# Performance work log

Measured on AMD Instinct MI355X. Metric: run time of the kernel, lower is better.

Reference implementation:

```python
import jax, jax.numpy as jnp
import numpy as np

D_MODEL = 2048
N_HEADS = 16
HEAD_DIM = D_MODEL // N_HEADS
CLIP_QKV = 6.0
LN_EPS = 1e-5


def _layernorm(x, g, b):
    mu = jnp.mean(x, axis=-1, keepdims=True)
    var = jnp.mean(jnp.square(x - mu), axis=-1, keepdims=True)
    return (x - mu) * jax.lax.rsqrt(var + LN_EPS) * g + b


def setup_inputs() -> dict:
    key = jax.random.key(0)
    ks = jax.random.split(key, 8)
    B, S = 2, 2048
    x = jax.random.normal(ks[0], (B, S, D_MODEL), dtype=jnp.float32)
    attn_bias = jax.random.normal(ks[1], (1, N_HEADS, 1, S), dtype=jnp.float32)
    key_padding_mask = jnp.ones((B, S), dtype=bool)
    Wqkv_w = jax.random.normal(ks[2], (3 * D_MODEL, D_MODEL), dtype=jnp.float32) * 0.02
    Wqkv_b = jnp.zeros((3 * D_MODEL,), dtype=jnp.float32)
    q_ln_g = jnp.ones((D_MODEL,), dtype=jnp.float32)
    q_ln_b = jnp.zeros((D_MODEL,), dtype=jnp.float32)
    k_ln_g = jnp.ones((D_MODEL,), dtype=jnp.float32)
    k_ln_b = jnp.zeros((D_MODEL,), dtype=jnp.float32)
    out_w = jax.random.normal(ks[3], (D_MODEL, D_MODEL), dtype=jnp.float32) * 0.02
    out_b = jnp.zeros((D_MODEL,), dtype=jnp.float32)
    return {
        'x': x, 'attn_bias': attn_bias, 'key_padding_mask': key_padding_mask,
        'Wqkv_w': Wqkv_w, 'Wqkv_b': Wqkv_b,
        'q_ln_g': q_ln_g, 'q_ln_b': q_ln_b, 'k_ln_g': k_ln_g, 'k_ln_b': k_ln_b,
        'out_w': out_w, 'out_b': out_b,
    }


def reference(x, attn_bias, key_padding_mask, Wqkv_w, Wqkv_b,
              q_ln_g, q_ln_b, k_ln_g, k_ln_b, out_w, out_b):
    B, S, _ = x.shape
    # Fused QKV projection + clip
    qkv = jnp.einsum('bsd,ed->bse', x, Wqkv_w) + Wqkv_b
    qkv = jnp.clip(qkv, -CLIP_QKV, CLIP_QKV)
    q, k, v = jnp.split(qkv, 3, axis=-1)
    # QK LayerNorm over full d_model
    q = _layernorm(q, q_ln_g, q_ln_b)
    k = _layernorm(k, k_ln_g, k_ln_b)
    # [b, s, d_model] -> [b, h, s, head_dim]
    q = q.reshape(B, S, N_HEADS, HEAD_DIM).transpose(0, 2, 1, 3)
    k = k.reshape(B, S, N_HEADS, HEAD_DIM).transpose(0, 2, 1, 3)
    v = v.reshape(B, S, N_HEADS, HEAD_DIM).transpose(0, 2, 1, 3)
    scale = 1.0 / np.sqrt(HEAD_DIM).astype(np.float32)
    scores = jnp.einsum('bhqd,bhkd->bhqk', q, k) * scale  # [b, h, s, s]
    scores = scores + attn_bias
    neg_inf = jnp.array(-jnp.inf, dtype=scores.dtype)
    scores = jnp.where(key_padding_mask[:, None, None, :], scores, neg_inf)
    causal = jnp.tril(jnp.ones((S, S), dtype=bool))
    scores = jnp.where(causal[None, None, :, :], scores, neg_inf)
    probs = jax.nn.softmax(scores, axis=-1)
    ctx = jnp.einsum('bhqk,bhkd->bhqd', probs, v)
    ctx = ctx.transpose(0, 2, 1, 3).reshape(B, S, D_MODEL)
    out = jnp.einsum('bsd,ed->bse', ctx, out_w) + out_b
    return out
```

## Files before the change

kernel.cpp:

```cpp
#include <hip/hip_runtime.h>

typedef unsigned short u16;
typedef unsigned int u32;
typedef __bf16 bf16x8 __attribute__((ext_vector_type(8)));
typedef float f32x4 __attribute__((ext_vector_type(4)));

#define DEV static __device__ __forceinline__

constexpr int D_MODEL = 2048;
constexpr int N_HEADS = 16;
constexpr int HEAD_DIM = 128;
constexpr int BB = 2;
constexpr int S = 2048;
constexpr int NTOK = BB * S;
constexpr int E3 = 3 * D_MODEL;
constexpr float CLIP_QKV = 6.0f;
constexpr float LN_EPS = 1e-5f;
constexpr float NEG_BIG = -30000.0f;

DEV u16 f2bf(float f) {
    u32 u = __float_as_uint(f);
    u = (u + 0x7FFFu + ((u >> 16) & 1u)) >> 16;
    return (u16)u;
}
DEV float bf2f(u16 h) { return __uint_as_float(((u32)h) << 16); }

DEV void stage8_f32(const float* __restrict__ src, u16* __restrict__ dst) {
    const float4 f0 = *reinterpret_cast<const float4*>(src);
    const float4 f1 = *reinterpret_cast<const float4*>(src + 4);
    u16 h[8] = {f2bf(f0.x), f2bf(f0.y), f2bf(f0.z), f2bf(f0.w),
                f2bf(f1.x), f2bf(f1.y), f2bf(f1.z), f2bf(f1.w)};
    *reinterpret_cast<uint4*>(dst) = *reinterpret_cast<const uint4*>(h);
}

DEV void gload16(const u16* g, u16* l) {
    __builtin_amdgcn_global_load_lds(
        (const __attribute__((address_space(1))) void*)g,
        (__attribute__((address_space(3))) void*)l, 16, 0, 0);
}

__global__ __launch_bounds__(256)
void k_cvt(const float* __restrict__ s, u16* __restrict__ d, int n8) {
    const int i = blockIdx.x * 256 + threadIdx.x;
    if (i < n8) stage8_f32(s + (size_t)i * 8, d + (size_t)i * 8);
}

template<bool DO_CLIP, bool OUT32>
__global__ __launch_bounds__(256)
void k_gemm_bt(const u16* __restrict__ A, const u16* __restrict__ Bm,
               const float* __restrict__ bias, void* __restrict__ Cp,
               int M, int N, int K) {
    __shared__ __align__(16) u16 As[128 * 32];
    __shared__ __align__(16) u16 Bs[128 * 32];

    const int tid = threadIdx.x;
    const int lane = tid & 63, w = tid >> 6;
    const int quad = lane >> 4, l16 = lane & 15;
    const int wm = w >> 1, wn = w & 1;
    const int m0 = blockIdx.y * 128, n0 = blockIdx.x * 128;

    f32x4 acc[4][4] = {};

    for (int k0 = 0; k0 < K; k0 += 32) {
        __syncthreads();
        #pragma unroll
        for (int j = 0; j < 2; ++j) {
            const int c = w * 128 + j * 64 + lane;
            const int row = c >> 2, cc = c & 3;
            gload16(A  + (size_t)(m0 + row) * K + k0 + cc * 8, &As[c * 8]);
            gload16(Bm + (size_t)(n0 + row) * K + k0 + cc * 8, &Bs[c * 8]);
        }
        __syncthreads();

        bf16x8 af[4], bfv[4];
        #pragma unroll
        for (int mt = 0; mt < 4; ++mt)
            af[mt] = *reinterpret_cast<const bf16x8*>(&As[(wm * 64 + mt * 16 + l16) * 32 + quad * 8]);
        #pragma unroll
        for (int nt = 0; nt < 4; ++nt)
            bfv[nt] = *reinterpret_cast<const bf16x8*>(&Bs[(wn * 64 + nt * 16 + l16) * 32 + quad * 8]);
        #pragma unroll
        for (int mt = 0; mt < 4; ++mt)
            #pragma unroll
            for (int nt = 0; nt < 4; ++nt)
                acc[mt][nt] = __builtin_amdgcn_mfma_f32_16x16x32_bf16(af[mt], bfv[nt], acc[mt][nt], 0, 0, 0);
    }

    #pragma unroll
    for (int mt = 0; mt < 4; ++mt) {
        const int row = m0 + wm * 64 + mt * 16 + quad * 4;
        #pragma unroll
        for (int nt = 0; nt < 4; ++nt) {
            const int col = n0 + wn * 64 + nt * 16 + l16;
            const float bv = bias[col];
            #pragma unroll
            for (int r = 0; r < 4; ++r) {
                float v = acc[mt][nt][r] + bv;
                if (DO_CLIP) v = fminf(CLIP_QKV, fmaxf(-CLIP_QKV, v));
                if (OUT32)
                    ((float*)Cp)[(size_t)(row + r) * N + col] = v;
                else
                    ((u16*)Cp)[(size_t)(row + r) * N + col] = f2bf(v);
            }
        }
    }
}

template<bool DO_CLIP, bool OUT32>
__global__ __launch_bounds__(512, 2)
void k_gemm256(const u16* __restrict__ A, const u16* __restrict__ Bm,
               const float* __restrict__ bias, void* __restrict__ Cp,
               int M, int N, int K) {
    __shared__ __align__(16) u16 lds[2][2][2][256 * 32];

    const int tid = threadIdx.x;
    const int lane = tid & 63, w = tid >> 6;
    const int quad = lane >> 4, l16 = lane & 15;
    const int wm = w >> 2, wn = w & 3;

    const int nwg = gridDim.x;
    const int bid = blockIdx.x;
    const int cpx = nwg >> 3;
    const int swz = (bid & 7) * cpx + (bid >> 3);
    const int gx = N >> 8;
    const int bx = swz % gx, by = swz / gx;
    const int m0 = by << 8, n0 = bx << 8;
    const int NT = K >> 6;

    u32 offA[2], offB[2];
    int loff[2];
    #pragma unroll
    for (int i = 0; i < 2; ++i) {
        const int c = i * 512 + w * 64 + lane;
        const int row = c >> 2;
        const int colb = ((c & 3) ^ ((row >> 1) & 3)) << 4;
        offA[i] = (u32)(m0 + row) * (u32)K + (u32)(colb >> 1);
        offB[i] = (u32)(n0 + row) * (u32)K + (u32)(colb >> 1);
        loff[i] = c * 8;
    }

    auto STAGE = [&](int buf, int op, int kh, int kt) {
        const u16* g = op ? Bm : A;
        const u32* of = op ? offB : offA;
        u16* l = lds[buf][op][kh];
        #pragma unroll
        for (int i = 0; i < 2; ++i)
            gload16(g + (size_t)of[i] + (size_t)(kt + kh * 32), l + loff[i]);
    };

    bf16x8 af[4], bfr[4];
    auto LDA = [&](int buf, int kh, int qm) {
        const u16* base = lds[buf][0][kh];
        #pragma unroll
        for (int mt = 0; mt < 4; ++mt) {
            const int row = wm * 128 + qm * 64 + mt * 16 + l16;
            af[mt] = *reinterpret_cast<const bf16x8*>(
                base + row * 32 + ((quad ^ ((row >> 1) & 3)) << 3));
        }
    };
    auto LDB = [&](int buf, int kh) {
        const u16* base = lds[buf][1][kh];
        #pragma unroll
        for (int nt = 0; nt < 4; ++nt) {
            const int row = wn * 64 + nt * 16 + l16;
            bfr[nt] = *reinterpret_cast<const bf16x8*>(
                base + row * 32 + ((quad ^ ((row >> 1) & 3)) << 3));
        }
    };

    f32x4 acc[2][4][4] = {};
    auto MM = [&](f32x4 (&ac)[4][4]) {
        __builtin_amdgcn_s_setprio(1);
        #pragma unroll
        for (int mt = 0; mt < 4; ++mt)
            #pragma unroll
            for (int nt = 0; nt < 4; ++nt)
                ac[mt][nt] = __builtin_amdgcn_mfma_f32_16x16x32_bf16(
                    af[mt], bfr[nt], ac[mt][nt], 0, 0, 0);
        __builtin_amdgcn_s_setprio(0);
    };

    STAGE(0, 0, 0, 0); STAGE(0, 1, 0, 0); STAGE(0, 0, 1, 0); STAGE(0, 1, 1, 0);
    if (NT > 1) {
        STAGE(1, 1, 0, 64); STAGE(1, 0, 0, 64); STAGE(1, 1, 1, 64);
        asm volatile("s_waitcnt vmcnt(6)" ::: "memory");
    } else {
        asm volatile("s_waitcnt vmcnt(0)" ::: "memory");
    }
    __builtin_amdgcn_s_barrier();
    __builtin_amdgcn_sched_barrier(0);

    for (int t = 0; t < NT; ++t) {
        const int p = t & 1;
        const int kt2 = (t + 2) << 6;

        LDA(p, 0, 0); LDB(p, 0);
        if (t + 1 < NT) STAGE(p ^ 1, 0, 1, (t + 1) << 6);
        __builtin_amdgcn_s_barrier();
        asm volatile("s_waitcnt lgkmcnt(0)");
        MM(acc[0]);
        __builtin_amdgcn_s_barrier();

        LDA(p, 0, 1);
        if (t + 2 < NT) STAGE(p, 1, 0, kt2);
        __builtin_amdgcn_s_barrier();
        asm volatile("s_waitcnt lgkmcnt(0)");
        MM(acc[1]);
        __builtin_amdgcn_s_barrier();

        LDA(p, 1, 0); LDB(p, 1);
        if (t + 2 < NT) STAGE(p, 0, 0, kt2);
        __builtin_amdgcn_s_barrier();
        asm volatile("s_waitcnt lgkmcnt(0)");
        MM(acc[0]);
        __builtin_amdgcn_s_barrier();

        LDA(p, 1, 1);
        if (t + 2 < NT) STAGE(p, 1, 1, kt2);
        __builtin_amdgcn_s_barrier();
        asm volatile("s_waitcnt lgkmcnt(0)");
        MM(acc[1]);
        if (t + 2 < NT)      asm volatile("s_waitcnt vmcnt(6)" ::: "memory");
        else if (t + 1 < NT) asm volatile("s_waitcnt vmcnt(0)" ::: "memory");
        __builtin_amdgcn_s_barrier();
        __builtin_amdgcn_sched_barrier(0);
    }

    #pragma unroll
    for (int qm = 0; qm < 2; ++qm)
        #pragma unroll
        for (int mt = 0; mt < 4; ++mt) {
            const int row = m0 + wm * 128 + qm * 64 + mt * 16 + quad * 4;
            #pragma unroll
            for (int nt = 0; nt < 4; ++nt) {
                const int col = n0 + wn * 64 + nt * 16 + l16;
                const float bv = bias[col];
                #pragma unroll
                for (int r = 0; r < 4; ++r) {
                    float v = acc[qm][mt][nt][r] + bv;
                    if (DO_CLIP) v = fminf(CLIP_QKV, fmaxf(-CLIP_QKV, v));
                    if (OUT32)
                        ((float*)Cp)[(size_t)(row + r) * N + col] = v;
                    else
                        ((u16*)Cp)[(size_t)(row + r) * N + col] = f2bf(v);
                }
            }
        }
}

__global__ __launch_bounds__(256)
void k_ln(const u16* __restrict__ qkvb,
          const float* __restrict__ gq, const float* __restrict__ bq,
          const float* __restrict__ gk, const float* __restrict__ bk,
          u16* __restrict__ qh, u16* __restrict__ kh) {
    __shared__ float red[8];
    const int tok = blockIdx.x;
    const int b = tok >> 11, s = tok & (S - 1);
    const int tid = threadIdx.x, lane = tid & 63, w = tid >> 6;

    #pragma unroll
    for (int part = 0; part < 2; ++part) {
        const int c0 = tid * 8;
        const u16* src = qkvb + (size_t)tok * E3 + part * D_MODEL + c0;
        u16 hx[8];
        *reinterpret_cast<uint4*>(hx) = *reinterpret_cast<const uint4*>(src);
        float x[8], sum = 0.f, sq = 0.f;
        #pragma unroll
        for (int j = 0; j < 8; ++j) { x[j] = bf2f(hx[j]); sum += x[j]; sq += x[j] * x[j]; }
        #pragma unroll
        for (int off = 1; off < 64; off <<= 1) {
            sum += __shfl_xor(sum, off, 64);
            sq  += __shfl_xor(sq,  off, 64);
        }
        __syncthreads();
        if (lane == 0) { red[w] = sum; red[4 + w] = sq; }
        __syncthreads();
        sum = red[0] + red[1] + red[2] + red[3];
        sq  = red[4] + red[5] + red[6] + red[7];
        const float mean = sum * (1.0f / D_MODEL);
        const float var  = fmaxf(sq * (1.0f / D_MODEL) - mean * mean, 0.0f);
        const float rstd = rsqrtf(var + LN_EPS);
        const float* g  = part ? gk : gq;
        const float* be = part ? bk : bq;
        u16 o[8];
        #pragma unroll
        for (int j = 0; j < 8; ++j)
            o[j] = f2bf((x[j] - mean) * rstd * g[c0 + j] + be[c0 + j]);
        const int h = c0 >> 7, d = c0 & (HEAD_DIM - 1);
        u16* dst = (part ? kh : qh) + ((size_t)((b * N_HEADS + h) * S + s)) * HEAD_DIM + d;
        *reinterpret_cast<uint4*>(dst) = *reinterpret_cast<uint4*>(o);
    }
}

__global__ __launch_bounds__(256)
void k_vtrans(const u16* __restrict__ qkvb, u16* __restrict__ vt) {
    constexpr int LDT = 136;
    __shared__ __align__(16) u16 tile[64 * LDT];
    const int blk = blockIdx.x;
    const int st = blk & 31, h = (blk >> 5) & 15, b = blk >> 9;
    const int s0 = st * 64;
    const int tid = threadIdx.x;

    #pragma unroll
    for (int i = 0; i < 4; ++i) {
        const int chunk = tid + i * 256;
        const int row = chunk >> 4, c8 = (chunk & 15) * 8;
        const u16* src = qkvb + (size_t)(b * S + s0 + row) * E3 + 2 * D_MODEL + h * HEAD_DIM + c8;
        *reinterpret_cast<uint4*>(&tile[row * LDT + c8]) = *reinterpret_cast<const uint4*>(src);
    }
    __syncthreads();
    #pragma unroll
    for (int i = 0; i < 4; ++i) {
        const int chunk = tid + i * 256;
        const int d = chunk >> 3, s8 = (chunk & 7) * 8;
        u16 o[8];
        #pragma unroll
        for (int j = 0; j < 8; ++j) o[j] = tile[(s8 + j) * LDT + d];
        u16* dst = vt + ((size_t)(b * N_HEADS + h) * HEAD_DIM + d) * S + s0 + s8;
        *reinterpret_cast<uint4*>(dst) = *reinterpret_cast<uint4*>(o);
    }
}

__global__ __launch_bounds__(256)
void k_attn(const u16* __restrict__ qh, const u16* __restrict__ kh,
            const u16* __restrict__ vt, const float* __restrict__ bias,
            u16* __restrict__ ctx) {
    constexpr int BQ = 128, BKV = 64;
    constexpr int LDK = 136;
    constexpr int LDV = 72;
    constexpr int LDP = 72;
    __shared__ __align__(16) u16 Ks[64 * LDK];
    __shared__ __align__(16) u16 Vs[128 * LDV];
    __shared__ __align__(16) u16 Ps[128 * LDP];

    const int blk = blockIdx.x;
    const int bh = blk & 31;
    const int qi = 15 - (blk >> 5);
    const int b = bh >> 4, h = bh & 15;
    const int q0 = qi * BQ;

    const int tid = threadIdx.x, lane = tid & 63, w = tid >> 6;
    const int quad = lane >> 4, l16 = lane & 15;

    const size_t bhS = (size_t)(b * N_HEADS + h) * S;
    const u16* Qt = qh + (bhS + q0) * HEAD_DIM;
    const u16* Kt = kh + bhS * HEAD_DIM;
    const u16* Vt = vt + (size_t)(b * N_HEADS + h) * HEAD_DIM * S;

    bf16x8 aq[2][4];
    #pragma unroll
    for (int mt = 0; mt < 2; ++mt)
        #pragma unroll
        for (int ks = 0; ks < 4; ++ks)
            aq[mt][ks] = *reinterpret_cast<const bf16x8*>(
                Qt + (size_t)(w * 32 + mt * 16 + l16) * HEAD_DIM + ks * 32 + quad * 8);

    f32x4 o[2][8] = {};
    float m_i[2][4], l_i[2][4];
    #pragma unroll
    for (int mt = 0; mt < 2; ++mt)
        #pragma unroll
        for (int r = 0; r < 4; ++r) { m_i[mt][r] = NEG_BIG; l_i[mt][r] = 0.f; }

    const float scale = 0.08838834764831845f;
    const int nkv = 2 * (qi + 1);

    for (int t = 0; t < nkv; ++t) {
        const int k0 = t * BKV;
        __syncthreads();
        #pragma unroll
        for (int i = 0; i < 4; ++i) {
            const int chunk = tid + i * 256;
            const int key = chunk >> 4, c8 = (chunk & 15) * 8;
            *reinterpret_cast<uint4*>(&Ks[key * LDK + c8]) =
                *reinterpret_cast<const uint4*>(Kt + (size_t)(k0 + key) * HEAD_DIM + c8);
        }
        #pragma unroll
        for (int i = 0; i < 4; ++i) {
            const int chunk = tid + i * 256;
            const int d = chunk >> 3, s8 = (chunk & 7) * 8;
            *reinterpret_cast<uint4*>(&Vs[d * LDV + s8]) =
                *reinterpret_cast<const uint4*>(Vt + (size_t)d * S + k0 + s8);
        }
        __syncthreads();

        f32x4 sc[2][4] = {};
        #pragma unroll
        for (int ks = 0; ks < 4; ++ks) {
            bf16x8 bk[4];
            #pragma unroll
            for (int nt = 0; nt < 4; ++nt)
                bk[nt] = *reinterpret_cast<const bf16x8*>(&Ks[(nt * 16 + l16) * LDK + ks * 32 + quad * 8]);
            #pragma unroll
            for (int mt = 0; mt < 2; ++mt)
                #pragma unroll
                for (int nt = 0; nt < 4; ++nt)
                    sc[mt][nt] = __builtin_amdgcn_mfma_f32_16x16x32_bf16(aq[mt][ks], bk[nt], sc[mt][nt], 0, 0, 0);
        }

        float bv[4];
        #pragma unroll
        for (int nt = 0; nt < 4; ++nt) bv[nt] = bias[h * S + k0 + nt * 16 + l16];
        const bool need_mask = (t >= 2 * qi);
        #pragma unroll
        for (int mt = 0; mt < 2; ++mt)
            #pragma unroll
            for (int nt = 0; nt < 4; ++nt) {
                const int kpos = k0 + nt * 16 + l16;
                #pragma unroll
                for (int r = 0; r < 4; ++r) {
                    float v = sc[mt][nt][r] * scale + bv[nt];
                    if (need_mask) {
                        const int qpos = q0 + w * 32 + mt * 16 + quad * 4 + r;
                        if (kpos > qpos) v = NEG_BIG;
                    }
                    sc[mt][nt][r] = v;
                }
            }

        #pragma unroll
        for (int mt = 0; mt < 2; ++mt)
            #pragma unroll
            for (int r = 0; r < 4; ++r) {
                float mx = fmaxf(fmaxf(sc[mt][0][r], sc[mt][1][r]), fmaxf(sc[mt][2][r], sc[mt][3][r]));
                mx = fmaxf(mx, __shfl_xor(mx, 1, 64));
                mx = fmaxf(mx, __shfl_xor(mx, 2, 64));
                mx = fmaxf(mx, __shfl_xor(mx, 4, 64));
                mx = fmaxf(mx, __shfl_xor(mx, 8, 64));
                const float mnew = fmaxf(m_i[mt][r], mx);
                const float alpha = __expf(m_i[mt][r] - mnew);
                float rs = 0.f;
                #pragma unroll
                for (int nt = 0; nt < 4; ++nt) {
                    const float p = __expf(sc[mt][nt][r] - mnew);
                    sc[mt][nt][r] = p;
                    rs += p;
                }
                rs += __shfl_xor(rs, 1, 64);
                rs += __shfl_xor(rs, 2, 64);
                rs += __shfl_xor(rs, 4, 64);
                rs += __shfl_xor(rs, 8, 64);
                l_i[mt][r] = l_i[mt][r] * alpha + rs;
                m_i[mt][r] = mnew;
                #pragma unroll
                for (int nt = 0; nt < 8; ++nt) o[mt][nt][r] *= alpha;
            }

        #pragma unroll
        for (int mt = 0; mt < 2; ++mt)
            #pragma unroll
            for (int nt = 0; nt < 4; ++nt)
                #pragma unroll
                for (int r = 0; r < 4; ++r)
                    Ps[(w * 32 + mt * 16 + quad * 4 + r) * LDP + nt * 16 + l16] = f2bf(sc[mt][nt][r]);

        __syncthreads();

        #pragma unroll
        for (int ks = 0; ks < 2; ++ks) {
            bf16x8 ap[2];
            #pragma unroll
            for (int mt = 0; mt < 2; ++mt)
                ap[mt] = *reinterpret_cast<const bf16x8*>(&Ps[(w * 32 + mt * 16 + l16) * LDP + ks * 32 + quad * 8]);
            #pragma unroll
            for (int nt = 0; nt < 8; ++nt) {
                const bf16x8 bvv = *reinterpret_cast<const bf16x8*>(&Vs[(nt * 16 + l16) * LDV + ks * 32 + quad * 8]);
                #pragma unroll
                for (int mt = 0; mt < 2; ++mt)
                    o[mt][nt] = __builtin_amdgcn_mfma_f32_16x16x32_bf16(ap[mt], bvv, o[mt][nt], 0, 0, 0);
            }
        }
    }

    #pragma unroll
    for (int mt = 0; mt < 2; ++mt)
        #pragma unroll
        for (int r = 0; r < 4; ++r) {
            const float inv_l = 1.0f / fmaxf(l_i[mt][r], 1e-20f);
            const int row = q0 + w * 32 + mt * 16 + quad * 4 + r;
            u16* dst = ctx + (size_t)(b * S + row) * D_MODEL + h * HEAD_DIM;
            #pragma unroll
            for (int nt = 0; nt < 8; ++nt)
                dst[nt * 16 + l16] = f2bf(o[mt][nt][r] * inv_l);
        }
}

extern "C" void kernel_launch(void* const* d_in, const int* in_sizes, int n_in,
                              void* d_out, int out_size, void* d_ws, size_t ws_size,
                              hipStream_t stream) {
    const float* x        = (const float*)d_in[0];
    const float* attn_bias= (const float*)d_in[1];
    const float* Wqkv_w   = (const float*)d_in[3];
    const float* Wqkv_b   = (const float*)d_in[4];
    const float* q_ln_g   = (const float*)d_in[5];
    const float* q_ln_b   = (const float*)d_in[6];
    const float* k_ln_g   = (const float*)d_in[7];
    const float* k_ln_b   = (const float*)d_in[8];
    const float* out_w    = (const float*)d_in[9];
    const float* out_b    = (const float*)d_in[10];

    char* ws = (char*)d_ws;
    u16* xb   = (u16*)ws; ws += (size_t)NTOK * D_MODEL * 2;
    u16* qkvb = (u16*)ws; ws += (size_t)NTOK * E3 * 2;
    u16* qhb  = (u16*)ws; ws += (size_t)NTOK * D_MODEL * 2;
    u16* khb  = (u16*)ws; ws += (size_t)NTOK * D_MODEL * 2;
    u16* vtb  = (u16*)ws; ws += (size_t)NTOK * D_MODEL * 2;
    u16* wqkvb = (u16*)d_out;
    u16* ctxb  = qkvb;
    u16* outwb = xb;

    k_cvt<<<(NTOK * D_MODEL / 8 + 255) / 256, 256, 0, stream>>>(x, xb, NTOK * D_MODEL / 8);
    k_cvt<<<(E3 * D_MODEL / 8 + 255) / 256, 256, 0, stream>>>(Wqkv_w, wqkvb, E3 * D_MODEL / 8);
    k_gemm256<true, false><<<(E3 / 256) * (NTOK / 256), 512, 0, stream>>>(
        xb, wqkvb, Wqkv_b, qkvb, NTOK, E3, D_MODEL);
    k_ln<<<NTOK, 256, 0, stream>>>(qkvb, q_ln_g, q_ln_b, k_ln_g, k_ln_b, qhb, khb);
    k_vtrans<<<BB * N_HEADS * (S / 64), 256, 0, stream>>>(qkvb, vtb);
    k_attn<<<BB * N_HEADS * (S / 128), 256, 0, stream>>>(qhb, khb, vtb, attn_bias, ctxb);
    k_cvt<<<(D_MODEL * D_MODEL / 8 + 255) / 256, 256, 0, stream>>>(out_w, outwb, D_MODEL * D_MODEL / 8);
    k_gemm_bt<false, true><<<dim3(D_MODEL / 128, NTOK / 128), 256, 0, stream>>>(
        ctxb, outwb, out_b, d_out, NTOK, D_MODEL, D_MODEL);
}
```

Before: 476.1 us.

## Prefetch next K/V tile into registers and cache bias in LDS

The attention kernel now issues the global loads for the next K/V tile into registers while the current tile is being computed, then writes them to shared memory at the start of the next iteration. This is meant to hide global-memory latency behind the MFMA work. It also stages the per-head bias row in LDS, drops the block barrier between the P write and the P read because each warp reads only its own rows, and requests an occupancy of 2 blocks per CU through launch bounds. The costs are extra registers for the prefetch buffers, which could cause spilling under the tighter launch bound, and 8 KB more shared memory per block.

Measured after the change: 583.3 us. +22.5%, slower.

```diff
diff --git a/kernel.cpp b/kernel.cpp
--- a/kernel.cpp
+++ b/kernel.cpp
@@ -321,7 +321,7 @@
     }
 }
 
-__global__ __launch_bounds__(256)
+__global__ __launch_bounds__(256, 2)
 void k_attn(const u16* __restrict__ qh, const u16* __restrict__ kh,
             const u16* __restrict__ vt, const float* __restrict__ bias,
             u16* __restrict__ ctx) {
@@ -332,6 +332,7 @@
     __shared__ __align__(16) u16 Ks[64 * LDK];
     __shared__ __align__(16) u16 Vs[128 * LDV];
     __shared__ __align__(16) u16 Ps[128 * LDP];
+    __shared__ __align__(16) float BiasS[S];
 
     const int blk = blockIdx.x;
     const int bh = blk & 31;
@@ -347,6 +348,13 @@
     const u16* Kt = kh + bhS * HEAD_DIM;
     const u16* Vt = vt + (size_t)(b * N_HEADS + h) * HEAD_DIM * S;
 
+    #pragma unroll
+    for (int i = 0; i < 2; ++i) {
+        const int j = tid * 4 + i * 1024;
+        *reinterpret_cast<float4*>(&BiasS[j]) =
+            *reinterpret_cast<const float4*>(&bias[h * S + j]);
+    }
+
     bf16x8 aq[2][4];
     #pragma unroll
     for (int mt = 0; mt < 2; ++mt)
@@ -365,24 +373,45 @@
     const float scale = 0.08838834764831845f;
     const int nkv = 2 * (qi + 1);
 
-    for (int t = 0; t < nkv; ++t) {
-        const int k0 = t * BKV;
-        __syncthreads();
+    uint4 kst[4], vst[4];
+    auto PFK = [&](int k0, uint4 (&kr)[4], uint4 (&vr)[4]) {
         #pragma unroll
         for (int i = 0; i < 4; ++i) {
             const int chunk = tid + i * 256;
             const int key = chunk >> 4, c8 = (chunk & 15) * 8;
-            *reinterpret_cast<uint4*>(&Ks[key * LDK + c8]) =
-                *reinterpret_cast<const uint4*>(Kt + (size_t)(k0 + key) * HEAD_DIM + c8);
+            kr[i] = *reinterpret_cast<const uint4*>(Kt + (size_t)(k0 + key) * HEAD_DIM + c8);
         }
         #pragma unroll
         for (int i = 0; i < 4; ++i) {
             const int chunk = tid + i * 256;
             const int d = chunk >> 3, s8 = (chunk & 7) * 8;
-            *reinterpret_cast<uint4*>(&Vs[d * LDV + s8]) =
-                *reinterpret_cast<const uint4*>(Vt + (size_t)d * S + k0 + s8);
-        }
-        __syncthreads();
+            vr[i] = *reinterpret_cast<const uint4*>(Vt + (size_t)d * S + k0 + s8);
+        }
+    };
+    PFK(0, kst, vst);
+
+    for (int t = 0; t < nkv; ++t) {
+        const int k0 = t * BKV;
+
+        #pragma unroll
+        for (int i = 0; i < 4; ++i) {
+            const int chunk = tid + i * 256;
+            const int key = chunk >> 4, c8 = (chunk & 15) * 8;
+            *reinterpret_cast<uint4*>(&Ks[key * LDK + c8]) = kst[i];
+        }
+        #pragma unroll
+        for (int i = 0; i < 4; ++i) {
+            const int chunk = tid + i * 256;
+            const int d = chunk >> 3, s8 = (chunk & 7) * 8;
+            *reinterpret_cast<uint4*>(&Vs[d * LDV + s8]) = vst[i];
+        }
+
+        const bool pf = (t + 1 < nkv);
+        uint4 knx[4], vnx[4];
+        if (pf) PFK(k0 + BKV, knx, vnx);
+
+        asm volatile("s_waitcnt lgkmcnt(0)" ::: "memory");
+        __builtin_amdgcn_s_barrier();
 
         f32x4 sc[2][4] = {};
         #pragma unroll
@@ -400,7 +429,7 @@
 
         float bv[4];
         #pragma unroll
-        for (int nt = 0; nt < 4; ++nt) bv[nt] = bias[h * S + k0 + nt * 16 + l16];
+        for (int nt = 0; nt < 4; ++nt) bv[nt] = BiasS[k0 + nt * 16 + l16];
         const bool need_mask = (t >= 2 * qi);
         #pragma unroll
         for (int mt = 0; mt < 2; ++mt)
@@ -454,7 +483,7 @@
                 for (int r = 0; r < 4; ++r)
                     Ps[(w * 32 + mt * 16 + quad * 4 + r) * LDP + nt * 16 + l16] = f2bf(sc[mt][nt][r]);
 
-        __syncthreads();
+        asm volatile("s_waitcnt lgkmcnt(0)" ::: "memory");
 
         #pragma unroll
         for (int ks = 0; ks < 2; ++ks) {
@@ -469,6 +498,13 @@
                 for (int mt = 0; mt < 2; ++mt)
                     o[mt][nt] = __builtin_amdgcn_mfma_f32_16x16x32_bf16(ap[mt], bvv, o[mt][nt], 0, 0, 0);
             }
+        }
+
+        __builtin_amdgcn_s_barrier();
+
+        if (pf) {
+            #pragma unroll
+            for (int i = 0; i < 4; ++i) { kst[i] = knx[i]; vst[i] = vnx[i]; }
         }
     }
 
```

## Prefetch next K/V tile into registers and drop redundant P barrier

Applied to the files above, without the earlier changes.

The attention kernel now loads the next K and V tiles from global memory into registers while the current tile is being computed. The registers are stored to shared memory at the start of the next iteration, so global-load latency overlaps with the MFMA work. The barrier between writing P and reading P is replaced by a local LDS wait, because each warp only reads back its own rows of P. A single barrier at the end of the loop now protects the K/V buffer before it is overwritten. A min-blocks hint of 2 is added to launch bounds, and the prefetch needs 32 extra VGPRs, which could cause register pressure or spills.

After: 485.2 us. About the same (+1.9%).

```diff
diff --git a/kernel.cpp b/kernel.cpp
--- a/kernel.cpp
+++ b/kernel.cpp
@@ -321,7 +321,7 @@
     }
 }
 
-__global__ __launch_bounds__(256)
+__global__ __launch_bounds__(256, 2)
 void k_attn(const u16* __restrict__ qh, const u16* __restrict__ kh,
             const u16* __restrict__ vt, const float* __restrict__ bias,
             u16* __restrict__ ctx) {
@@ -347,6 +347,9 @@
     const u16* Kt = kh + bhS * HEAD_DIM;
     const u16* Vt = vt + (size_t)(b * N_HEADS + h) * HEAD_DIM * S;
 
+    const int kkey = tid >> 4, kc8 = (tid & 15) * 8;
+    const int vd = tid >> 3, vs8 = (tid & 7) * 8;
+
     bf16x8 aq[2][4];
     #pragma unroll
     for (int mt = 0; mt < 2; ++mt)
@@ -365,24 +368,53 @@
     const float scale = 0.08838834764831845f;
     const int nkv = 2 * (qi + 1);
 
+    uint4 ka0, ka1, ka2, ka3, va0, va1, va2, va3;
+    {
+        const u16* kp = Kt + (size_t)kkey * HEAD_DIM + kc8;
+        ka0 = *reinterpret_cast<const uint4*>(kp);
+        ka1 = *reinterpret_cast<const uint4*>(kp + 16 * HEAD_DIM);
+        ka2 = *reinterpret_cast<const uint4*>(kp + 32 * HEAD_DIM);
+        ka3 = *reinterpret_cast<const uint4*>(kp + 48 * HEAD_DIM);
+        const u16* vp = Vt + (size_t)vd * S + vs8;
+        va0 = *reinterpret_cast<const uint4*>(vp);
+        va1 = *reinterpret_cast<const uint4*>(vp + (size_t)32 * S);
+        va2 = *reinterpret_cast<const uint4*>(vp + (size_t)64 * S);
+        va3 = *reinterpret_cast<const uint4*>(vp + (size_t)96 * S);
+    }
+
     for (int t = 0; t < nkv; ++t) {
         const int k0 = t * BKV;
-        __syncthreads();
-        #pragma unroll
-        for (int i = 0; i < 4; ++i) {
-            const int chunk = tid + i * 256;
-            const int key = chunk >> 4, c8 = (chunk & 15) * 8;
-            *reinterpret_cast<uint4*>(&Ks[key * LDK + c8]) =
-                *reinterpret_cast<const uint4*>(Kt + (size_t)(k0 + key) * HEAD_DIM + c8);
-        }
-        #pragma unroll
-        for (int i = 0; i < 4; ++i) {
-            const int chunk = tid + i * 256;
-            const int d = chunk >> 3, s8 = (chunk & 7) * 8;
-            *reinterpret_cast<uint4*>(&Vs[d * LDV + s8]) =
-                *reinterpret_cast<const uint4*>(Vt + (size_t)d * S + k0 + s8);
-        }
-        __syncthreads();
+
+        {
+            u16* kd = &Ks[kkey * LDK + kc8];
+            *reinterpret_cast<uint4*>(kd)            = ka0;
+            *reinterpret_cast<uint4*>(kd + 16 * LDK) = ka1;
+            *reinterpret_cast<uint4*>(kd + 32 * LDK) = ka2;
+            *reinterpret_cast<uint4*>(kd + 48 * LDK) = ka3;
+            u16* vdst = &Vs[vd * LDV + vs8];
+            *reinterpret_cast<uint4*>(vdst)            = va0;
+            *reinterpret_cast<uint4*>(vdst + 32 * LDV) = va1;
+            *reinterpret_cast<uint4*>(vdst + 64 * LDV) = va2;
+            *reinterpret_cast<uint4*>(vdst + 96 * LDV) = va3;
+        }
+
+        const bool pf = (t + 1 < nkv);
+        uint4 kb0, kb1, kb2, kb3, vb0, vb1, vb2, vb3;
+        if (pf) {
+            const u16* kp = Kt + (size_t)(k0 + BKV + kkey) * HEAD_DIM + kc8;
+            kb0 = *reinterpret_cast<const uint4*>(kp);
+            kb1 = *reinterpret_cast<const uint4*>(kp + 16 * HEAD_DIM);
+            kb2 = *reinterpret_cast<const uint4*>(kp + 32 * HEAD_DIM);
+            kb3 = *reinterpret_cast<const uint4*>(kp + 48 * HEAD_DIM);
+            const u16* vp = Vt + (size_t)vd * S + k0 + BKV + vs8;
+            vb0 = *reinterpret_cast<const uint4*>(vp);
+            vb1 = *reinterpret_cast<const uint4*>(vp + (size_t)32 * S);
+            vb2 = *reinterpret_cast<const uint4*>(vp + (size_t)64 * S);
+            vb3 = *reinterpret_cast<const uint4*>(vp + (size_t)96 * S);
+        }
+
+        asm volatile("s_waitcnt lgkmcnt(0)" ::: "memory");
+        __builtin_amdgcn_s_barrier();
 
         f32x4 sc[2][4] = {};
         #pragma unroll
@@ -454,7 +486,7 @@
                 for (int r = 0; r < 4; ++r)
                     Ps[(w * 32 + mt * 16 + quad * 4 + r) * LDP + nt * 16 + l16] = f2bf(sc[mt][nt][r]);
 
-        __syncthreads();
+        asm volatile("s_waitcnt lgkmcnt(0)" ::: "memory");
 
         #pragma unroll
         for (int ks = 0; ks < 2; ++ks) {
@@ -469,6 +501,13 @@
                 for (int mt = 0; mt < 2; ++mt)
                     o[mt][nt] = __builtin_amdgcn_mfma_f32_16x16x32_bf16(ap[mt], bvv, o[mt][nt], 0, 0, 0);
             }
+        }
+
+        __builtin_amdgcn_s_barrier();
+
+        if (pf) {
+            ka0 = kb0; ka1 = kb1; ka2 = kb2; ka3 = kb3;
+            va0 = vb0; va1 = vb1; va2 = vb2; va3 = vb3;
         }
     }
 
```
